# Kernel tuning notes

Hardware: AMD Instinct MI355X
Metric: run time of the kernel (lower is better)

## Reference

```python
import jax, jax.numpy as jnp
import numpy as np
from jax import lax

N_NEURONS = 256
N_EDGES = 1024
BATCH = 128
HW = 28
KSIZE = 5
FC_HID = 200
N_CLS = 10


def _make_graph():
    # Replicates the torch __init__ random incidence construction; retries seeds
    # until the last neuron is reachable from neuron 0 (else torch forward loops forever).
    for seed in range(1000):
        rng = np.random.default_rng(seed)
        src = np.zeros(N_EDGES, np.int32)
        tgt = np.zeros(N_EDGES, np.int32)
        for e in range(N_EDGES):
            t = int(rng.choice(np.arange(1, N_NEURONS)))
            pool = np.arange(0, N_NEURONS - 1)
            if t < N_NEURONS - 1:
                pool = np.delete(pool, t)  # np.delete(range(0,N-1), target) as in source
            src[e] = int(rng.choice(pool))
            tgt[e] = t
        processed = np.zeros(N_NEURONS, bool)
        processed[0] = True
        frontier = [0]
        while frontier and not processed[-1]:
            nxt = set()
            for v in frontier:
                for m in tgt[src == v]:
                    if not processed[m]:
                        nxt.add(int(m))
            for m in nxt:
                processed[m] = True
            frontier = sorted(nxt)
        if processed[-1]:
            return src, tgt
    raise RuntimeError('no reachable graph found')


def _schedule(src, tgt, n):
    # Ordered input list per neuron (edge order, as np.where gives) + BFS waves from neuron 0.
    in_lists = [list(src[np.where(tgt == i)[0]]) for i in range(n)]
    waves = []
    processed = np.zeros(n, bool)
    frontier = [0]
    while True:
        waves.append(list(frontier))
        processed[frontier] = True
        if processed[n - 1]:
            break
        nxt = set()
        for v in frontier:
            for m in tgt[src == v]:
                if not processed[m]:
                    nxt.add(int(m))
        frontier = sorted(nxt)
        assert frontier, 'last neuron unreachable'
    return in_lists, waves


def setup_inputs() -> dict:
    src, tgt = _make_graph()
    rng = np.random.default_rng(123)
    deg = np.bincount(tgt, minlength=N_NEURONS)
    in_count = np.maximum(deg, 1)  # torch forces input_count>=1
    cmax = int(in_count.max())
    fan = np.sqrt(in_count.astype(np.float32) * KSIZE * KSIZE)
    conv_w = rng.normal(size=(N_NEURONS, 1, cmax, KSIZE, KSIZE)).astype(np.float32)
    conv_w /= fan[:, None, None, None, None]
    # zero out padding channels beyond each neuron's true in_count
    mask = (np.arange(cmax)[None, :] < in_count[:, None]).astype(np.float32)
    conv_w *= mask[:, None, :, None, None]
    conv_b = (0.01 * rng.normal(size=(N_NEURONS,))).astype(np.float32)
    deg_last = int(in_count[-1])
    fc1_w = (rng.normal(size=(FC_HID, deg_last * HW * HW)) / np.sqrt(deg_last * HW * HW)).astype(np.float32)
    fc1_b = np.zeros(FC_HID, np.float32)
    fc2_w = (rng.normal(size=(N_CLS, FC_HID)) / np.sqrt(FC_HID)).astype(np.float32)
    fc2_b = np.zeros(N_CLS, np.float32)
    x = jax.random.normal(jax.random.key(0), (BATCH, 1, HW, HW), jnp.float32)
    return {'x': x, 'src': jnp.asarray(src), 'tgt': jnp.asarray(tgt),
            'conv_w': jnp.asarray(conv_w), 'conv_b': jnp.asarray(conv_b),
            'fc1_w': jnp.asarray(fc1_w), 'fc1_b': jnp.asarray(fc1_b),
            'fc2_w': jnp.asarray(fc2_w), 'fc2_b': jnp.asarray(fc2_b)}


def _conv(g, w):  # g: [B,C,H,W], w: [1,C,5,5] -> [B,1,H,W], SAME padding 2
    return lax.conv_general_dilated(g, w, (1, 1), [(2, 2), (2, 2)])


def reference(x, src, tgt, conv_w, conv_b, fc1_w, fc1_b, fc2_w, fc2_b):
    src_np = np.asarray(src)
    tgt_np = np.asarray(tgt)
    n = int(conv_w.shape[0])
    cmax = int(conv_w.shape[2])
    B, H = x.shape[0], x.shape[2]
    in_lists, waves = _schedule(src_np, tgt_np, n)
    idx_pad = np.zeros((n, cmax), np.int32)  # pad idx 0 is safe: padded weight channels are zero
    for i, lst in enumerate(in_lists):
        idx_pad[i, :len(lst)] = lst

    out = jnp.zeros((n, B, H, H), x.dtype)  # per-neuron activations (unprocessed stay zero)
    hidden = None
    for wi, wave in enumerate(waves):
        snap = out  # within a wave, neurons read the previous wave's outputs
        if wi == 0:
            o0 = jax.nn.relu(_conv(x, conv_w[0, :, :1])[:, 0] + conv_b[0])
            out = out.at[0].set(o0)
            continue
        conv_nodes = [v for v in wave if v != n - 1]
        if conv_nodes:
            cn = jnp.asarray(np.array(conv_nodes, np.int32))
            g = snap[idx_pad[conv_nodes]]        # [K, Cmax, B, H, H]
            g = g.transpose(0, 2, 1, 3, 4)       # [K, B, Cmax, H, H]
            res = jax.vmap(_conv)(g, conv_w[cn])  # [K, B, 1, H, H]
            res = jax.nn.relu(res[:, :, 0] + conv_b[cn][:, None, None, None])
            out = out.at[cn].set(res)
        if (n - 1) in wave:
            lst = np.array(in_lists[n - 1], np.int32)
            comp = snap[lst].transpose(1, 0, 2, 3).reshape(B, -1)  # cat along channel then flatten
            hidden = jax.nn.relu(comp @ fc1_w.T + fc1_b)
    logits = hidden @ fc2_w.T + fc2_b
    return jax.nn.log_softmax(logits, axis=1)
```

## Files before the change

kernel.cpp:

```cpp
#include <hip/hip_runtime.h>

#define N_NEUR 256
#define N_EDGE 1024
#define BATCH  128
#define HWDIM  28
#define IMG    784
#define FCH    200
#define NCLS   10
#define INF_W  0x3fffffff
#define SLOTS  257
#define XSLOT  256
#define TSZ    1024
#define NT1    1024
#define NWAVE  16
#define HROWS  18

#define ACT_FLOATS ((size_t)BATCH * SLOTS * TSZ)

__global__ __launch_bounds__(NT1, 4)
void conv_kernel(const float* __restrict__ x, const int* __restrict__ src,
                 const int* __restrict__ tgt, const float* __restrict__ conv_w,
                 const float* __restrict__ conv_b, float* __restrict__ act,
                 int* __restrict__ gsched, int cmax)
{
    const int tid = threadIdx.x;
    const int b   = blockIdx.x;

    __shared__ float s_half[NWAVE][2][HROWS * 32];
    __shared__ int   s_off[N_NEUR + 2];
    __shared__ int   s_dat[N_EDGE];
    __shared__ int   s_wn[N_NEUR];
    __shared__ int   s_wo[N_NEUR + 2];
    __shared__ int   s_na[N_NEUR];
    __shared__ int   s_W;
    __shared__ int   s_done;

    int* e_src = (int*)&s_half[0][0][0];
    int* e_tgt = e_src + N_EDGE;
    int* wv    = e_tgt + N_EDGE;

    if (tid < N_EDGE) { e_src[tid] = src[tid]; e_tgt[tid] = tgt[tid]; }
    if (tid < N_NEUR) wv[tid] = (tid == 0) ? 0 : INF_W;
    __syncthreads();
    for (int w = 0; w < N_NEUR; ++w) {
        if (tid == 0) s_done = (wv[N_NEUR - 1] != INF_W);
        __syncthreads();
        if (s_done) break;
        {
            int s = e_src[tid], t = e_tgt[tid];
            if (wv[s] == w && wv[t] == INF_W) wv[t] = w + 1;
        }
        __syncthreads();
    }
    if (tid < N_NEUR) {
        int na = 0;
        const int wvv = wv[tid];
        for (int e = 0; e < N_EDGE; ++e)
            if (e_tgt[e] == tid && wv[e_src[e]] < wvv) ++na;
        if (tid == 0) na = 1;
        s_na[tid] = na;
    }
    __syncthreads();
    if (tid == 0) {
        int o = 0;
        for (int v = 0; v < N_NEUR; ++v) { s_off[v] = o; o += s_na[v]; }
        s_off[N_NEUR] = o;
        s_W = wv[N_NEUR - 1];
    }
    __syncthreads();
    if (tid < N_NEUR) {
        if (tid == 0) {
            s_dat[s_off[0]] = XSLOT;
        } else {
            int o = s_off[tid], c = 0;
            const int wvv = wv[tid];
            for (int e = 0; e < N_EDGE; ++e) {
                if (e_tgt[e] == tid) {
                    if (wv[e_src[e]] < wvv) s_dat[o++] = e_src[e] | (c << 9);
                    ++c;
                }
            }
        }
    }
    __syncthreads();
    {
        const int Wl = s_W;
        if (tid <= Wl + 1) {
            int cn = 0;
            for (int v2 = 0; v2 < N_NEUR - 1; ++v2) if (wv[v2] < tid) ++cn;
            s_wo[tid] = cn;
        }
        if (tid < N_NEUR - 1 && wv[tid] <= Wl) {
            int pos = 0; const int mw = wv[tid];
            for (int v2 = 0; v2 < N_NEUR - 1; ++v2) {
                int w2 = wv[v2];
                if (w2 < mw || (w2 == mw && v2 < tid)) ++pos;
            }
            s_wn[pos] = tid;
        }
    }
    __syncthreads();
    {
        const int naL = s_off[N_NEUR] - s_off[N_NEUR - 1];
        if (tid == 0) gsched[0] = naL;
        if (tid < naL) gsched[1 + tid] = s_dat[s_off[N_NEUR - 1] + tid];
    }
    for (int u = tid; u < SLOTS * 72; u += NT1) {
        const int t = u % 72, tile = u / 72;
        float* tp = act + (((size_t)b * SLOTS + tile) << 10);
        if (t < 16) {
            int eb = (t < 8) ? t * 8 : 960 + (t - 8) * 8;
            float4 z = make_float4(0.f, 0.f, 0.f, 0.f);
            ((float4*)(tp + eb))[0] = z; ((float4*)(tp + eb))[1] = z;
        } else {
            int s = t - 16;
            int eb = (2 + (s >> 1)) * 32 + ((s & 1) ? 30 : 0);
            *((float2*)(tp + eb)) = make_float2(0.f, 0.f);
        }
    }
    for (int u = tid; u < 196; u += NT1) {
        const int row = u / 7, col = (u - row * 7) * 4;
        float4 v4 = *(const float4*)(x + b * IMG + row * HWDIM + col);
        float* tp = act + (((size_t)b * SLOTS + XSLOT) << 10) + (row + 2) * 32 + col + 2;
        *(float2*)tp       = make_float2(v4.x, v4.y);
        *(float2*)(tp + 2) = make_float2(v4.z, v4.w);
    }
    __syncthreads();

    const int wid  = tid >> 6;
    const int lane = tid & 63;
    const int half = wid & 1;
    const int rs   = half * 14;
    const bool la  = lane < 49;
    const int cy   = lane / 7, cx = lane - 7 * (lane / 7);
    float* bufA = &s_half[wid][0][0];
    float* bufB = &s_half[wid][1][0];

    auto loadStg = [&](float4* st, int oo) {
        const int uu = __builtin_amdgcn_readfirstlane(s_dat[oo]) & 511;
        const float4* gs = (const float4*)(act + (((size_t)b * SLOTS + uu) << 10)) + rs * 8;
        st[0] = gs[lane];
        st[1] = gs[lane + 64];
        if (lane < 16) st[2] = gs[lane + 128];
    };
    auto storeLds = [&](float* buf, const float4* st) {
        float4* b4 = (float4*)buf;
        {
            const int fl = lane, lr = fl >> 3, cg = fl & 7;
            b4[(lr << 3) | (cg ^ ((lr >> 2) & 7))] = st[0];
        }
        {
            const int fl = lane + 64, lr = fl >> 3, cg = fl & 7;
            b4[(lr << 3) | (cg ^ ((lr >> 2) & 7))] = st[1];
        }
        if (lane < 16) {
            const int fl = lane + 128, lr = fl >> 3, cg = fl & 7;
            b4[(lr << 3) | (cg ^ ((lr >> 2) & 7))] = st[2];
        }
    };

    for (int w = 0; w <= s_W; ++w) {
        for (int ni2 = 2 * s_wo[w] + wid; ni2 < 2 * s_wo[w + 1]; ni2 += NWAVE) {
            const int ni = ni2 >> 1;
            const int v  = __builtin_amdgcn_readfirstlane(s_wn[ni]);
            const int o0 = s_off[v], o1 = s_off[v + 1];
            const float bias = conv_b[v];
            float acc[8];
            #pragma unroll
            for (int k = 0; k < 8; ++k) acc[k] = bias;

            float4 stgA[3], stgB[3];
            float  wgA[25], wgB[25];
            loadStg(stgA, o0);
            if (o0 + 1 < o1) loadStg(stgB, o0 + 1);
            {
                const int pk = __builtin_amdgcn_readfirstlane(s_dat[o0]);
                const float* wp = conv_w + ((size_t)v * cmax + (pk >> 9)) * 25;
                #pragma unroll
                for (int k = 0; k < 25; ++k) wgA[k] = wp[k];
            }

            auto computeBuf = [&](const float* buf, const float* wg) {
                if (!la) return;
                const float4* b4 = (const float4*)buf;
                #pragma unroll
                for (int r = 0; r < 6; ++r) {
                    const int lr = 2 * cy + r;
                    const int sw = (lr >> 2) & 7;
                    float4 fa = b4[(lr << 3) | (cx ^ sw)];
                    float4 fb = b4[(lr << 3) | ((cx + 1) ^ sw)];
                    const float f[8] = {fa.x, fa.y, fa.z, fa.w, fb.x, fb.y, fb.z, fb.w};
                    #pragma unroll
                    for (int i = 0; i < 2; ++i) {
                        const int tr = r - i;
                        if (tr < 0 || tr > 4) continue;
                        #pragma unroll
                        for (int dx = 0; dx < 5; ++dx) {
                            const float wvv = wg[tr * 5 + dx];
                            #pragma unroll
                            for (int j = 0; j < 4; ++j)
                                acc[i * 4 + j] = fmaf(f[j + dx], wvv, acc[i * 4 + j]);
                        }
                    }
                }
            };

            int o = o0;
            while (true) {
                storeLds(bufA, stgA);
                if (o + 2 < o1) loadStg(stgA, o + 2);
                if (o + 1 < o1) {
                    const int pk = __builtin_amdgcn_readfirstlane(s_dat[o + 1]);
                    const float* wp = conv_w + ((size_t)v * cmax + (pk >> 9)) * 25;
                    #pragma unroll
                    for (int k = 0; k < 25; ++k) wgB[k] = wp[k];
                }
                computeBuf(bufA, wgA);
                ++o; if (o >= o1) break;
                storeLds(bufB, stgB);
                if (o + 2 < o1) loadStg(stgB, o + 2);
                if (o + 1 < o1) {
                    const int pk = __builtin_amdgcn_readfirstlane(s_dat[o + 1]);
                    const float* wp = conv_w + ((size_t)v * cmax + (pk >> 9)) * 25;
                    #pragma unroll
                    for (int k = 0; k < 25; ++k) wgA[k] = wp[k];
                }
                computeBuf(bufB, wgB);
                ++o; if (o >= o1) break;
            }

            if (la) {
                float* gd = act + (((size_t)b * SLOTS + v) << 10);
                #pragma unroll
                for (int i = 0; i < 2; ++i) {
                    float* p = gd + (rs + 2 + 2 * cy + i) * 32 + 2 + 4 * cx;
                    *(float2*)p       = make_float2(fmaxf(acc[i*4+0], 0.f), fmaxf(acc[i*4+1], 0.f));
                    *(float2*)(p + 2) = make_float2(fmaxf(acc[i*4+2], 0.f), fmaxf(acc[i*4+3], 0.f));
                }
            }
        }
        __syncthreads();
    }
}

#define FC1_BT 16
#define FC1_HT 16
#define FC1_STRIDE 900

__global__ __launch_bounds__(256, 2)
void fc1_kernel(const float* __restrict__ act, const float* __restrict__ fc1_w,
                const float* __restrict__ fc1_b, float* __restrict__ hidden,
                const int* __restrict__ gsched, int dlast)
{
    const int tid = threadIdx.x;
    const int bt  = blockIdx.x & 7;
    const int ht  = blockIdx.x >> 3;
    const int b0  = bt * FC1_BT;
    const int h0  = ht * FC1_HT;
    __shared__ float s_act[FC1_BT * FC1_STRIDE];
    const int naL = gsched[0];
    const int bb  = tid & 15, hh = tid >> 4;
    const int h   = h0 + hh;
    float acc = 0.f;

    for (int a = 0; a < naL; ++a) {
        const int pk = gsched[1 + a];
        const int u = pk & 511, k = pk >> 9;
        __syncthreads();
        for (int idx = tid; idx < FC1_BT * 224; idx += 256) {
            const int bi = idx / 224, rr = idx - bi * 224;
            const int r = rr >> 3, cg = rr & 7;
            const float4 vv = *((const float4*)(act +
                (((size_t)(b0 + bi) * SLOTS + u) << 10) + (r + 2) * 32) + cg);
            *(float4*)(&s_act[bi * FC1_STRIDE + r * 32 + cg * 4]) = vv;
        }
        __syncthreads();
        if (h < FCH) {
            const float* wrow = fc1_w + (size_t)h * ((size_t)dlast * IMG) + (size_t)k * IMG;
            const float* Tb   = &s_act[bb * FC1_STRIDE];
            for (int r = 0; r < HWDIM; ++r) {
                const float4* w4 = (const float4*)(wrow + r * HWDIM);
                const float*  tr = Tb + r * 32 + 2;
                #pragma unroll
                for (int q = 0; q < 7; ++q) {
                    const float4 wv = w4[q];
                    acc = fmaf(tr[4*q+0], wv.x, acc);
                    acc = fmaf(tr[4*q+1], wv.y, acc);
                    acc = fmaf(tr[4*q+2], wv.z, acc);
                    acc = fmaf(tr[4*q+3], wv.w, acc);
                }
            }
        }
    }
    if (h < FCH) hidden[(b0 + bb) * FCH + h] = fmaxf(acc + fc1_b[h], 0.f);
}

__global__ __launch_bounds__(128, 1)
void fc2_kernel(const float* __restrict__ hidden, const float* __restrict__ fc2_w,
                const float* __restrict__ fc2_b, float* __restrict__ dout)
{
    const int b = threadIdx.x;
    float hr[FCH];
    const float* hp = hidden + b * FCH;
    for (int h = 0; h < FCH; h += 2) {
        float2 v2 = *(const float2*)(hp + h);
        hr[h] = v2.x; hr[h + 1] = v2.y;
    }
    float lg[NCLS], m = -1e30f;
    #pragma unroll
    for (int c = 0; c < NCLS; ++c) {
        float a2 = fc2_b[c];
        const float* wr = fc2_w + c * FCH;
        for (int hh = 0; hh < FCH; ++hh) a2 = fmaf(hr[hh], wr[hh], a2);
        lg[c] = a2;
        m = fmaxf(m, a2);
    }
    float s = 0.0f;
    #pragma unroll
    for (int c = 0; c < NCLS; ++c) s += expf(lg[c] - m);
    const float ls = m + logf(s);
    #pragma unroll
    for (int c = 0; c < NCLS; ++c) dout[b * NCLS + c] = lg[c] - ls;
}

extern "C" void kernel_launch(void* const* d_in, const int* in_sizes, int n_in,
                              void* d_out, int out_size, void* d_ws, size_t ws_size,
                              hipStream_t stream) {
    const float* x      = (const float*)d_in[0];
    const int*   src    = (const int*)d_in[1];
    const int*   tgt    = (const int*)d_in[2];
    const float* conv_w = (const float*)d_in[3];
    const float* conv_b = (const float*)d_in[4];
    const float* fc1_w  = (const float*)d_in[5];
    const float* fc1_b  = (const float*)d_in[6];
    const float* fc2_w  = (const float*)d_in[7];
    const float* fc2_b  = (const float*)d_in[8];
    float* out = (float*)d_out;
    float* ws  = (float*)d_ws;

    const int cmax  = in_sizes[3] / (N_NEUR * 25);
    const int dlast = in_sizes[5] / (FCH * IMG);

    float* act    = ws;
    float* hidden = ws + ACT_FLOATS;
    int*   gsched = (int*)(hidden + BATCH * FCH);

    hipLaunchKernelGGL(conv_kernel, dim3(BATCH), dim3(NT1), 0, stream,
                       x, src, tgt, conv_w, conv_b, act, gsched, cmax);
    hipLaunchKernelGGL(fc1_kernel, dim3(104), dim3(256), 0, stream,
                       act, fc1_w, fc1_b, hidden, gsched, dlast);
    hipLaunchKernelGGL(fc2_kernel, dim3(1), dim3(128), 0, stream,
                       hidden, fc2_w, fc2_b, out);
}
```

Before: 327.2 us.

## Process whole 28x28 neuron per wavefront instead of splitting rows across two waves

Each wavefront now computes a full neuron output (4 output rows x 4 cols per lane, 16 accumulators) rather than two wavefronts splitting it into 14-row halves. It stages the full 1024-float padded tile in LDS, doubling LDS per wavefront, and reorders the weight prefetch to sit after compute with sched_barriers. The aim is to halve the redundant halo loads and the per-neuron overhead. In exchange, parallelism per wave level drops by half, register pressure rises and LDS occupancy is tighter.

```diff
diff --git a/kernel.cpp b/kernel.cpp
--- a/kernel.cpp
+++ b/kernel.cpp
@@ -13,7 +13,6 @@
 #define TSZ    1024
 #define NT1    1024
 #define NWAVE  16
-#define HROWS  18
 
 #define ACT_FLOATS ((size_t)BATCH * SLOTS * TSZ)
 
@@ -26,7 +25,7 @@
     const int tid = threadIdx.x;
     const int b   = blockIdx.x;
 
-    __shared__ float s_half[NWAVE][2][HROWS * 32];
+    __shared__ float s_tiles[NWAVE][2][TSZ];
     __shared__ int   s_off[N_NEUR + 2];
     __shared__ int   s_dat[N_EDGE];
     __shared__ int   s_wn[N_NEUR];
@@ -35,7 +34,7 @@
     __shared__ int   s_W;
     __shared__ int   s_done;
 
-    int* e_src = (int*)&s_half[0][0][0];
+    int* e_src = (int*)&s_tiles[0][0][0];
     int* e_tgt = e_src + N_EDGE;
     int* wv    = e_tgt + N_EDGE;
 
@@ -129,69 +128,72 @@
 
     const int wid  = tid >> 6;
     const int lane = tid & 63;
-    const int half = wid & 1;
-    const int rs   = half * 14;
     const bool la  = lane < 49;
     const int cy   = lane / 7, cx = lane - 7 * (lane / 7);
-    float* bufA = &s_half[wid][0][0];
-    float* bufB = &s_half[wid][1][0];
+    float* bufA = &s_tiles[wid][0][0];
+    float* bufB = &s_tiles[wid][1][0];
 
     auto loadStg = [&](float4* st, int oo) {
         const int uu = __builtin_amdgcn_readfirstlane(s_dat[oo]) & 511;
-        const float4* gs = (const float4*)(act + (((size_t)b * SLOTS + uu) << 10)) + rs * 8;
-        st[0] = gs[lane];
-        st[1] = gs[lane + 64];
-        if (lane < 16) st[2] = gs[lane + 128];
+        const float4* gs = (const float4*)(act + (((size_t)b * SLOTS + uu) << 10));
+        #pragma unroll
+        for (int i = 0; i < 4; ++i) st[i] = gs[lane + 64 * i];
     };
+    auto loadWg = [&](float* wg, int oo) {
+        const int pk = __builtin_amdgcn_readfirstlane(s_dat[oo]);
+        const int v2 = __builtin_amdgcn_readfirstlane(s_wn[0]);
+        (void)v2;
+        return pk;
+    };
+    (void)loadWg;
     auto storeLds = [&](float* buf, const float4* st) {
         float4* b4 = (float4*)buf;
-        {
-            const int fl = lane, lr = fl >> 3, cg = fl & 7;
-            b4[(lr << 3) | (cg ^ ((lr >> 2) & 7))] = st[0];
-        }
-        {
-            const int fl = lane + 64, lr = fl >> 3, cg = fl & 7;
-            b4[(lr << 3) | (cg ^ ((lr >> 2) & 7))] = st[1];
-        }
-        if (lane < 16) {
-            const int fl = lane + 128, lr = fl >> 3, cg = fl & 7;
-            b4[(lr << 3) | (cg ^ ((lr >> 2) & 7))] = st[2];
+        #pragma unroll
+        for (int i = 0; i < 4; ++i) {
+            const int fl = lane + 64 * i;
+            const int lr = fl >> 3, cg = fl & 7;
+            b4[(lr << 3) | (cg ^ ((lr >> 2) & 7))] = st[i];
         }
     };
 
     for (int w = 0; w <= s_W; ++w) {
-        for (int ni2 = 2 * s_wo[w] + wid; ni2 < 2 * s_wo[w + 1]; ni2 += NWAVE) {
-            const int ni = ni2 >> 1;
+        for (int ni = s_wo[w] + wid; ni < s_wo[w + 1]; ni += NWAVE) {
             const int v  = __builtin_amdgcn_readfirstlane(s_wn[ni]);
             const int o0 = s_off[v], o1 = s_off[v + 1];
             const float bias = conv_b[v];
-            float acc[8];
+            float acc[16];
             #pragma unroll
-            for (int k = 0; k < 8; ++k) acc[k] = bias;
-
-            float4 stgA[3], stgB[3];
-            float  wgA[25], wgB[25];
-            loadStg(stgA, o0);
-            if (o0 + 1 < o1) loadStg(stgB, o0 + 1);
+            for (int k = 0; k < 16; ++k) acc[k] = bias;
+
+            float4 sA[4], sB[4];
+            float  wA[25], wB[25];
+            loadStg(sA, o0);
             {
                 const int pk = __builtin_amdgcn_readfirstlane(s_dat[o0]);
                 const float* wp = conv_w + ((size_t)v * cmax + (pk >> 9)) * 25;
                 #pragma unroll
-                for (int k = 0; k < 25; ++k) wgA[k] = wp[k];
+                for (int k = 0; k < 25; ++k) wA[k] = wp[k];
+            }
+            if (o0 + 1 < o1) {
+                loadStg(sB, o0 + 1);
+                const int pk = __builtin_amdgcn_readfirstlane(s_dat[o0 + 1]);
+                const float* wp = conv_w + ((size_t)v * cmax + (pk >> 9)) * 25;
+                #pragma unroll
+                for (int k = 0; k < 25; ++k) wB[k] = wp[k];
             }
 
             auto computeBuf = [&](const float* buf, const float* wg) {
                 if (!la) return;
                 const float4* b4 = (const float4*)buf;
                 #pragma unroll
-                for (int r = 0; r < 6; ++r) {
-                    const int lr = 2 * cy + r;
-                    const int sw = (lr >> 2) & 7;
-                    float4 fa = b4[(lr << 3) | (cx ^ sw)];
-                    float4 fb = b4[(lr << 3) | ((cx + 1) ^ sw)];
+                for (int r = 0; r < 8; ++r) {
+                    const int row = 4 * cy + r;
+                    const int sw  = (row >> 2) & 7;
+                    float4 fa = b4[(row << 3) | (cx ^ sw)];
+                    float4 fb = b4[(row << 3) | ((cx + 1) ^ sw)];
                     const float f[8] = {fa.x, fa.y, fa.z, fa.w, fb.x, fb.y, fb.z, fb.w};
                     #pragma unroll
-                    for (int i = 0; i < 2; ++i) {
+                    for (int i = 0; i < 4; ++i) {
                         const int tr = r - i;
                         if (tr < 0 || tr > 4) continue;
                         #pragma unroll
@@ -207,33 +209,35 @@
 
             int o = o0;
             while (true) {
-                storeLds(bufA, stgA);
-                if (o + 2 < o1) loadStg(stgA, o + 2);
-                if (o + 1 < o1) {
-                    const int pk = __builtin_amdgcn_readfirstlane(s_dat[o + 1]);
+                storeLds(bufA, sA);
+                if (o + 2 < o1) loadStg(sA, o + 2);
+                __builtin_amdgcn_sched_barrier(0);
+                computeBuf(bufA, wA);
+                if (o + 2 < o1) {
+                    const int pk = __builtin_amdgcn_readfirstlane(s_dat[o + 2]);
                     const float* wp = conv_w + ((size_t)v * cmax + (pk >> 9)) * 25;
                     #pragma unroll
-                    for (int k = 0; k < 25; ++k) wgB[k] = wp[k];
-                }
-                computeBuf(bufA, wgA);
+                    for (int k = 0; k < 25; ++k) wA[k] = wp[k];
+                }
                 ++o; if (o >= o1) break;
-                storeLds(bufB, stgB);
-                if (o + 2 < o1) loadStg(stgB, o + 2);
-                if (o + 1 < o1) {
-                    const int pk = __builtin_amdgcn_readfirstlane(s_dat[o + 1]);
+                storeLds(bufB, sB);
+                if (o + 2 < o1) loadStg(sB, o + 2);
+                __builtin_amdgcn_sched_barrier(0);
+                computeBuf(bufB, wB);
+                if (o + 2 < o1) {
+                    const int pk = __builtin_amdgcn_readfirstlane(s_dat[o + 2]);
                     const float* wp = conv_w + ((size_t)v * cmax + (pk >> 9)) * 25;
                     #pragma unroll
-                    for (int k = 0; k < 25; ++k) wgA[k] = wp[k];
-                }
-                computeBuf(bufB, wgB);
+                    for (int k = 0; k < 25; ++k) wB[k] = wp[k];
+                }
                 ++o; if (o >= o1) break;
             }
 
             if (la) {
                 float* gd = act + (((size_t)b * SLOTS + v) << 10);
                 #pragma unroll
-                for (int i = 0; i < 2; ++i) {
-                    float* p = gd + (rs + 2 + 2 * cy + i) * 32 + 2 + 4 * cx;
+                for (int i = 0; i < 4; ++i) {
+                    float* p = gd + (2 + 4 * cy + i) * 32 + 2 + 4 * cx;
                     *(float2*)p       = make_float2(fmaxf(acc[i*4+0], 0.f), fmaxf(acc[i*4+1], 0.f));
                     *(float2*)(p + 2) = make_float2(fmaxf(acc[i*4+2], 0.f), fmaxf(acc[i*4+3], 0.f));
                 }
```

Result: slower. 349.3 us (+6.7%).
